# Kernel optimization log

Measured on AMD Instinct MI355X. Metric: run time of the kernel, lower is better.

## Reference

```python
import jax, jax.numpy as jnp
from jax import lax
import numpy as np

KERNEL_NUM = 6
KERNEL_SIZES = [3 + 2 * i for i in range(KERNEL_NUM)]  # 3,5,7,9,11,13
DN = ('NCHW', 'OIHW', 'NCHW')


def _conv3x3(x, W, b):
    y = lax.conv_general_dilated(x, W, (1, 1), [(1, 1), (1, 1)], dimension_numbers=DN)
    return y + b[None, :, None, None]


def _box_sum(x, k):
    # x: (N, 1, H, W); all-ones kxk conv with zero padding (k-1)//2, as in convSs[i]
    p = (k - 1) // 2
    kern = jnp.ones((1, 1, k, k), x.dtype)
    return lax.conv_general_dilated(x, kern, (1, 1), [(p, p), (p, p)], dimension_numbers=DN)


def _gamma(x):
    # bmfr_gamma_correction: clamp to >=0, then pow(1/2.2)
    return jnp.power(jnp.maximum(x, 0.0), jnp.float32(1.0 / 2.2))


def setup_inputs() -> dict:
    key = jax.random.key(0)
    ks = jax.random.split(key, 7)
    B, C, H, W = 2, 10, 1080, 1920
    s = 0.1
    return {
        'x_in': jax.random.uniform(ks[0], (B, C, H, W), jnp.float32),
        'W1': jax.random.normal(ks[1], (14, 10, 3, 3), jnp.float32) * s,
        'b1': jnp.zeros((14,), jnp.float32),
        'W2': jax.random.normal(ks[2], (14, 14, 3, 3), jnp.float32) * s,
        'b2': jnp.zeros((14,), jnp.float32),
        'W3': jax.random.normal(ks[3], (12, 14, 3, 3), jnp.float32) * s,
        'b3': jnp.zeros((12,), jnp.float32),
    }


def reference(x_in, W1, b1, W2, b2, W3, b3):
    irr = x_in[:, 0:3]
    alb = x_in[:, 3:6]
    x_inputs = jnp.concatenate([_gamma(irr * alb), x_in[:, 3:]], axis=1)  # (B,10,H,W)
    # RepVGG([10,14,14,12]) (deploy form): 3x3 convs, ReLU between, linear output
    h = jax.nn.relu(_conv3x3(x_inputs, W1, b1))
    h = jax.nn.relu(_conv3x3(h, W2, b2))
    out = _conv3x3(h, W3, b3)  # (B,12,H,W)
    guide = jnp.exp(out[:, :KERNEL_NUM])           # (B,6,H,W)
    alpha = jax.nn.softmax(out[:, KERNEL_NUM:], axis=1)  # Softmax2d over channels
    B, _, H, W = x_inputs.shape
    x_out = jnp.zeros((B, 3, H, W), x_in.dtype)
    for i, k in enumerate(KERNEL_SIZES):
        g = guide[:, i:i + 1]                                  # (B,1,H,W)
        wsum = _box_sum(g, k)                                  # (B,1,H,W)
        num = _box_sum((g * irr).reshape(-1, 1, H, W), k).reshape(B, 3, H, W)
        x_out = x_out + alpha[:, i:i + 1] * (num / wsum)
    return x_out * alb
```

## Files before the change

kernel.cpp:

```cpp
#include <hip/hip_runtime.h>
#include <math.h>

namespace {

constexpr int BATCH = 2;
constexpr int H = 1080;
constexpr int W = 1920;
constexpr int HW = H * W;
constexpr int PL = BATCH * HW;
constexpr int NTH = 256;

constexpr int BX = 128;
constexpr int BY = 8;
constexpr int LW = 132;
constexpr int LH = 10;
constexpr int LDSN = LW * LH;
constexpr int NSTG = (LDSN + NTH - 1) / NTH;

constexpr int RMAX = 6;
constexpr int SW_B = 240;
constexpr int COLS = SW_B + 2 * RMAX;
constexpr int SH_B = 4;

__device__ __forceinline__ float gamma22(float v) {
    return v > 0.f ? exp2f(0.45454545454545453f * log2f(v)) : 0.f;
}

template<int CIN, int COUT, bool GAMMA, bool RELU, bool HEAD>
__global__ __launch_bounds__(NTH) void conv4_k(
        const float* __restrict__ in, const float* __restrict__ wgt,
        const float* __restrict__ bias, float* __restrict__ out)
{
    __shared__ float tile[LDSN];

    const int tx = threadIdx.x & 31;
    const int ty = threadIdx.x >> 5;
    const int x0 = blockIdx.x * BX;
    const int y0 = blockIdx.y * BY;
    const int b  = blockIdx.z;

    float acc[COUT][4];
#pragma unroll
    for (int co = 0; co < COUT; ++co) {
        float bv = bias[co];
#pragma unroll
        for (int p = 0; p < 4; ++p) acc[co][p] = bv;
    }

    float rg[NSTG];

    auto stage_load = [&](int ci) {
#pragma unroll
        for (int s = 0; s < NSTG; ++s) {
            int i = threadIdx.x + s * NTH;
            float v = 0.f;
            if (i < LDSN) {
                int r = i / LW, c = i - r * LW;
                int gy = y0 + r - 1, gx = x0 + c - 1;
                if (c < 130 && gy >= 0 && gy < H && gx >= 0 && gx < W) {
                    if (GAMMA) {
                        if (ci < 3) {
                            float a  = in[((size_t)b * 10 + ci) * HW + (size_t)gy * W + gx];
                            float al = in[((size_t)b * 10 + ci + 3) * HW + (size_t)gy * W + gx];
                            v = gamma22(a * al);
                        } else {
                            v = in[((size_t)b * 10 + ci) * HW + (size_t)gy * W + gx];
                        }
                    } else {
                        v = in[(size_t)ci * PL + (size_t)b * HW + (size_t)gy * W + gx];
                    }
                }
            }
            rg[s] = v;
        }
    };

    stage_load(0);

    for (int ci = 0; ci < CIN; ++ci) {
        __syncthreads();
#pragma unroll
        for (int s = 0; s < NSTG; ++s) {
            int i = threadIdx.x + s * NTH;
            if (i < LDSN) tile[i] = rg[s];
        }
        __syncthreads();

        if (ci + 1 < CIN) stage_load(ci + 1);

        float v[3][6];
#pragma unroll
        for (int ky = 0; ky < 3; ++ky) {
            int row = (ty + ky) * LW + tx * 4;
            float4 vA = *reinterpret_cast<const float4*>(&tile[row]);
            float4 vB = *reinterpret_cast<const float4*>(&tile[row + 4]);
            v[ky][0] = vA.x; v[ky][1] = vA.y; v[ky][2] = vA.z; v[ky][3] = vA.w;
            v[ky][4] = vB.x; v[ky][5] = vB.y;
        }

#pragma unroll
        for (int ky = 0; ky < 3; ++ky) {
#pragma unroll
            for (int kx = 0; kx < 3; ++kx) {
#pragma unroll
                for (int co = 0; co < COUT; ++co) {
                    float w = wgt[(co * CIN + ci) * 9 + ky * 3 + kx];
#pragma unroll
                    for (int p = 0; p < 4; ++p)
                        acc[co][p] = fmaf(v[ky][p + kx], w, acc[co][p]);
                }
            }
        }
    }

    const int y = y0 + ty;
    const size_t obase = (size_t)b * HW + (size_t)y * W + x0 + tx * 4;

    if (HEAD) {
#pragma unroll
        for (int p = 0; p < 4; ++p) {
#pragma unroll
            for (int c = 0; c < 6; ++c)
                out[(size_t)c * PL + obase + p] = expf(acc[c][p]);
            float m = acc[6][p];
#pragma unroll
            for (int c = 7; c < 12; ++c) m = fmaxf(m, acc[c][p]);
            float e[6]; float s = 0.f;
#pragma unroll
            for (int c = 0; c < 6; ++c) { e[c] = expf(acc[6 + c][p] - m); s += e[c]; }
            float inv = 1.f / s;
#pragma unroll
            for (int c = 0; c < 6; ++c)
                out[(size_t)(6 + c) * PL + obase + p] = e[c] * inv;
        }
    } else {
#pragma unroll
        for (int co = 0; co < COUT; ++co) {
            float4 r;
            r.x = RELU ? fmaxf(acc[co][0], 0.f) : acc[co][0];
            r.y = RELU ? fmaxf(acc[co][1], 0.f) : acc[co][1];
            r.z = RELU ? fmaxf(acc[co][2], 0.f) : acc[co][2];
            r.w = RELU ? fmaxf(acc[co][3], 0.f) : acc[co][3];
            *reinterpret_cast<float4*>(&out[(size_t)co * PL + obase]) = r;
        }
    }
}

__global__ __launch_bounds__(NTH) void box_all_k(
        const float* __restrict__ ga, const float* __restrict__ xin,
        float* __restrict__ outp)
{
    __shared__ float4 vls4[6 * NTH];

    const int t  = threadIdx.x;
    const int x0 = blockIdx.x * SW_B;
    const int y0 = blockIdx.y * SH_B;
    const int b  = blockIdx.z;
    const int x  = x0 - RMAX + t;

    const bool tok = t < COLS;
    const bool xok = tok && x >= 0 && x < W;
    const bool ook = t >= RMAX && t < RMAX + SW_B;

    const float* gb = ga + (size_t)b * HW;
    const float* xb = xin + (size_t)b * 10 * HW;

    float vs[6][4];
#pragma unroll
    for (int i = 0; i < 6; ++i)
#pragma unroll
        for (int c = 0; c < 4; ++c) vs[i][c] = 0.f;

#pragma unroll
    for (int r = -RMAX; r <= RMAX; ++r) {
        int yy = y0 + r;
        float g[6], ir[3];
        if (xok && yy >= 0 && yy < H) {
            size_t ro = (size_t)yy * W + x;
#pragma unroll
            for (int i = 0; i < 6; ++i) g[i] = gb[(size_t)i * PL + ro];
#pragma unroll
            for (int c = 0; c < 3; ++c) ir[c] = xb[(size_t)c * HW + ro];
        } else {
#pragma unroll
            for (int i = 0; i < 6; ++i) g[i] = 0.f;
#pragma unroll
            for (int c = 0; c < 3; ++c) ir[c] = 0.f;
        }
#pragma unroll
        for (int i = 0; i < 6; ++i) {
            if (r >= -(i + 1) && r <= (i + 1)) {
                vs[i][0] += g[i];
                vs[i][1] = fmaf(g[i], ir[0], vs[i][1]);
                vs[i][2] = fmaf(g[i], ir[1], vs[i][2]);
                vs[i][3] = fmaf(g[i], ir[2], vs[i][3]);
            }
        }
    }

    for (int dy = 0; dy < SH_B; ++dy) {
        const int y = y0 + dy;
        const size_t ro = (size_t)y * W + x;

        float al[6], ab[3];
        if (ook) {
#pragma unroll
            for (int i = 0; i < 6; ++i) al[i] = gb[(size_t)(6 + i) * PL + ro];
#pragma unroll
            for (int c = 0; c < 3; ++c) ab[c] = xb[(size_t)(3 + c) * HW + ro];
        }

        if (tok) {
#pragma unroll
            for (int i = 0; i < 6; ++i)
                vls4[i * NTH + t] = make_float4(vs[i][0], vs[i][1], vs[i][2], vs[i][3]);
        }
        __syncthreads();

        if (dy + 1 < SH_B && xok) {
#pragma unroll
            for (int i = 0; i < 6; ++i) {
                const int R = i + 1;
                int ya = y + 1 + R;
                int yr = y - R;
                if (ya < H) {
                    size_t r2 = (size_t)ya * W + x;
                    float g = gb[(size_t)i * PL + r2];
                    vs[i][0] += g;
                    vs[i][1] = fmaf(g, xb[r2], vs[i][1]);
                    vs[i][2] = fmaf(g, xb[(size_t)HW + r2], vs[i][2]);
                    vs[i][3] = fmaf(g, xb[(size_t)2 * HW + r2], vs[i][3]);
                }
                if (yr >= 0) {
                    size_t r2 = (size_t)yr * W + x;
                    float g = gb[(size_t)i * PL + r2];
                    vs[i][0] -= g;
                    vs[i][1] = fmaf(-g, xb[r2], vs[i][1]);
                    vs[i][2] = fmaf(-g, xb[(size_t)HW + r2], vs[i][2]);
                    vs[i][3] = fmaf(-g, xb[(size_t)2 * HW + r2], vs[i][3]);
                }
            }
        }

        if (ook) {
            float o0 = 0.f, o1 = 0.f, o2 = 0.f;
#pragma unroll
            for (int i = 0; i < 6; ++i) {
                const int R = i + 1;
                float sw = 0.f, s0 = 0.f, s1 = 0.f, s2 = 0.f;
#pragma unroll
                for (int dx = -R; dx <= R; ++dx) {
                    float4 v = vls4[i * NTH + t + dx];
                    sw += v.x; s0 += v.y; s1 += v.z; s2 += v.w;
                }
                float rw = al[i] / sw;
                o0 = fmaf(s0, rw, o0);
                o1 = fmaf(s1, rw, o1);
                o2 = fmaf(s2, rw, o2);
            }
            size_t o = (size_t)b * 3 * HW + ro;
            outp[o]                  = o0 * ab[0];
            outp[o + HW]             = o1 * ab[1];
            outp[o + (size_t)2 * HW] = o2 * ab[2];
        }
        __syncthreads();
    }
}

}

extern "C" void kernel_launch(void* const* d_in, const int* in_sizes, int n_in,
                              void* d_out, int out_size, void* d_ws, size_t ws_size,
                              hipStream_t stream)
{
    const float* xin = (const float*)d_in[0];
    const float* W1p = (const float*)d_in[1];
    const float* b1p = (const float*)d_in[2];
    const float* W2p = (const float*)d_in[3];
    const float* b2p = (const float*)d_in[4];
    const float* W3p = (const float*)d_in[5];
    const float* b3p = (const float*)d_in[6];
    float* outp = (float*)d_out;
    float* ws = (float*)d_ws;

    float* h1 = ws;
    float* h2 = ws + (size_t)14 * PL;
    float* ga = ws;

    dim3 blk(NTH);
    dim3 cgrid(W / BX, H / BY, BATCH);
    dim3 bgrid(W / SW_B, H / SH_B, BATCH);

    conv4_k<10, 14, true,  true,  false><<<cgrid, blk, 0, stream>>>(xin, W1p, b1p, h1);
    conv4_k<14, 14, false, true,  false><<<cgrid, blk, 0, stream>>>(h1,  W2p, b2p, h2);
    conv4_k<14, 12, false, false, true ><<<cgrid, blk, 0, stream>>>(h2,  W3p, b3p, ga);

    box_all_k<<<bgrid, blk, 0, stream>>>(ga, xin, outp);
}
```

Baseline: 661.4 us.

## Widen conv tiles to eight pixels per thread and load box-filter guides only when used

The three 3x3 conv kernels now compute 8 horizontal pixels per thread over a 256-wide tile instead of 4 over 128. This halves LDS reads and weight loads per FMA. Because 1920 is not a multiple of 256, the grid is rounded up and half the threads in the last column of blocks do no useful work, guarded by an early return before the stores. Accumulator registers double, which may lower occupancy. The box-filter kernel now loads each guide channel only for the rows inside that channel's window, which cuts redundant global loads in the outer rows.

```diff
diff --git a/kernel.cpp b/kernel.cpp
--- a/kernel.cpp
+++ b/kernel.cpp
@@ -10,9 +10,9 @@
 constexpr int PL = BATCH * HW;
 constexpr int NTH = 256;
 
-constexpr int BX = 128;
+constexpr int BX = 256;
 constexpr int BY = 8;
-constexpr int LW = 132;
+constexpr int LW = 260;
 constexpr int LH = 10;
 constexpr int LDSN = LW * LH;
 constexpr int NSTG = (LDSN + NTH - 1) / NTH;
@@ -27,7 +27,7 @@
 }
 
 template<int CIN, int COUT, bool GAMMA, bool RELU, bool HEAD>
-__global__ __launch_bounds__(NTH) void conv4_k(
+__global__ __launch_bounds__(NTH) void conv8_k(
         const float* __restrict__ in, const float* __restrict__ wgt,
         const float* __restrict__ bias, float* __restrict__ out)
 {
@@ -39,12 +39,14 @@
     const int y0 = blockIdx.y * BY;
     const int b  = blockIdx.z;
 
-    float acc[COUT][4];
+    const bool sok = x0 + tx * 8 < W;
+
+    float acc[COUT][8];
 #pragma unroll
     for (int co = 0; co < COUT; ++co) {
         float bv = bias[co];
 #pragma unroll
-        for (int p = 0; p < 4; ++p) acc[co][p] = bv;
+        for (int p = 0; p < 8; ++p) acc[co][p] = bv;
     }
 
     float rg[NSTG];
@@ -57,7 +59,7 @@
             if (i < LDSN) {
                 int r = i / LW, c = i - r * LW;
                 int gy = y0 + r - 1, gx = x0 + c - 1;
-                if (c < 130 && gy >= 0 && gy < H && gx >= 0 && gx < W) {
+                if (c < 258 && gy >= 0 && gy < H && gx >= 0 && gx < W) {
                     if (GAMMA) {
                         if (ci < 3) {
                             float a  = in[((size_t)b * 10 + ci) * HW + (size_t)gy * W + gx];
@@ -88,14 +90,16 @@
 
         if (ci + 1 < CIN) stage_load(ci + 1);
 
-        float v[3][6];
+        float v[3][12];
 #pragma unroll
         for (int ky = 0; ky < 3; ++ky) {
-            int row = (ty + ky) * LW + tx * 4;
+            int row = (ty + ky) * LW + tx * 8;
             float4 vA = *reinterpret_cast<const float4*>(&tile[row]);
             float4 vB = *reinterpret_cast<const float4*>(&tile[row + 4]);
-            v[ky][0] = vA.x; v[ky][1] = vA.y; v[ky][2] = vA.z; v[ky][3] = vA.w;
-            v[ky][4] = vB.x; v[ky][5] = vB.y;
+            float4 vC = *reinterpret_cast<const float4*>(&tile[row + 8]);
+            v[ky][0] = vA.x; v[ky][1]  = vA.y; v[ky][2]  = vA.z; v[ky][3]  = vA.w;
+            v[ky][4] = vB.x; v[ky][5]  = vB.y; v[ky][6]  = vB.z; v[ky][7]  = vB.w;
+            v[ky][8] = vC.x; v[ky][9]  = vC.y; v[ky][10] = vC.z; v[ky][11] = vC.w;
         }
 
 #pragma unroll
@@ -106,19 +110,20 @@
                 for (int co = 0; co < COUT; ++co) {
                     float w = wgt[(co * CIN + ci) * 9 + ky * 3 + kx];
 #pragma unroll
-                    for (int p = 0; p < 4; ++p)
+                    for (int p = 0; p < 8; ++p)
                         acc[co][p] = fmaf(v[ky][p + kx], w, acc[co][p]);
                 }
             }
         }
     }
 
+    if (!sok) return;
     const int y = y0 + ty;
-    const size_t obase = (size_t)b * HW + (size_t)y * W + x0 + tx * 4;
+    const size_t obase = (size_t)b * HW + (size_t)y * W + x0 + tx * 8;
 
     if (HEAD) {
 #pragma unroll
-        for (int p = 0; p < 4; ++p) {
+        for (int p = 0; p < 8; ++p) {
 #pragma unroll
             for (int c = 0; c < 6; ++c)
                 out[(size_t)c * PL + obase + p] = expf(acc[c][p]);
@@ -136,12 +141,17 @@
     } else {
 #pragma unroll
         for (int co = 0; co < COUT; ++co) {
-            float4 r;
-            r.x = RELU ? fmaxf(acc[co][0], 0.f) : acc[co][0];
-            r.y = RELU ? fmaxf(acc[co][1], 0.f) : acc[co][1];
-            r.z = RELU ? fmaxf(acc[co][2], 0.f) : acc[co][2];
-            r.w = RELU ? fmaxf(acc[co][3], 0.f) : acc[co][3];
-            *reinterpret_cast<float4*>(&out[(size_t)co * PL + obase]) = r;
+            float4 r0, r1;
+            r0.x = RELU ? fmaxf(acc[co][0], 0.f) : acc[co][0];
+            r0.y = RELU ? fmaxf(acc[co][1], 0.f) : acc[co][1];
+            r0.z = RELU ? fmaxf(acc[co][2], 0.f) : acc[co][2];
+            r0.w = RELU ? fmaxf(acc[co][3], 0.f) : acc[co][3];
+            r1.x = RELU ? fmaxf(acc[co][4], 0.f) : acc[co][4];
+            r1.y = RELU ? fmaxf(acc[co][5], 0.f) : acc[co][5];
+            r1.z = RELU ? fmaxf(acc[co][6], 0.f) : acc[co][6];
+            r1.w = RELU ? fmaxf(acc[co][7], 0.f) : acc[co][7];
+            *reinterpret_cast<float4*>(&out[(size_t)co * PL + obase])     = r0;
+            *reinterpret_cast<float4*>(&out[(size_t)co * PL + obase + 4]) = r1;
         }
     }
 }
@@ -174,26 +184,22 @@
 #pragma unroll
     for (int r = -RMAX; r <= RMAX; ++r) {
         int yy = y0 + r;
-        float g[6], ir[3];
-        if (xok && yy >= 0 && yy < H) {
-            size_t ro = (size_t)yy * W + x;
-#pragma unroll
-            for (int i = 0; i < 6; ++i) g[i] = gb[(size_t)i * PL + ro];
-#pragma unroll
-            for (int c = 0; c < 3; ++c) ir[c] = xb[(size_t)c * HW + ro];
-        } else {
-#pragma unroll
-            for (int i = 0; i < 6; ++i) g[i] = 0.f;
-#pragma unroll
-            for (int c = 0; c < 3; ++c) ir[c] = 0.f;
+        const bool rowok = xok && yy >= 0 && yy < H;
+        size_t ro = (size_t)yy * W + x;
+        float ir0 = 0.f, ir1 = 0.f, ir2 = 0.f;
+        if (rowok) {
+            ir0 = xb[ro];
+            ir1 = xb[(size_t)HW + ro];
+            ir2 = xb[(size_t)2 * HW + ro];
         }
 #pragma unroll
         for (int i = 0; i < 6; ++i) {
             if (r >= -(i + 1) && r <= (i + 1)) {
-                vs[i][0] += g[i];
-                vs[i][1] = fmaf(g[i], ir[0], vs[i][1]);
-                vs[i][2] = fmaf(g[i], ir[1], vs[i][2]);
-                vs[i][3] = fmaf(g[i], ir[2], vs[i][3]);
+                float g = rowok ? gb[(size_t)i * PL + ro] : 0.f;
+                vs[i][0] += g;
+                vs[i][1] = fmaf(g, ir0, vs[i][1]);
+                vs[i][2] = fmaf(g, ir1, vs[i][2]);
+                vs[i][3] = fmaf(g, ir2, vs[i][3]);
             }
         }
     }
@@ -288,12 +294,12 @@
     float* ga = ws;
 
     dim3 blk(NTH);
-    dim3 cgrid(W / BX, H / BY, BATCH);
+    dim3 cgrid((W + BX - 1) / BX, H / BY, BATCH);
     dim3 bgrid(W / SW_B, H / SH_B, BATCH);
 
-    conv4_k<10, 14, true,  true,  false><<<cgrid, blk, 0, stream>>>(xin, W1p, b1p, h1);
-    conv4_k<14, 14, false, true,  false><<<cgrid, blk, 0, stream>>>(h1,  W2p, b2p, h2);
-    conv4_k<14, 12, false, false, true ><<<cgrid, blk, 0, stream>>>(h2,  W3p, b3p, ga);
+    conv8_k<10, 14, true,  true,  false><<<cgrid, blk, 0, stream>>>(xin, W1p, b1p, h1);
+    conv8_k<14, 14, false, true,  false><<<cgrid, blk, 0, stream>>>(h1,  W2p, b2p, h2);
+    conv8_k<14, 12, false, false, true ><<<cgrid, blk, 0, stream>>>(h2,  W3p, b3p, ga);
 
     box_all_k<<<bgrid, blk, 0, stream>>>(ga, xin, outp);
 }
```

Result: slower. 999.1 us (+51.1%).
